# Kernel optimization log

Measured on AMD Instinct MI355X. Metric: run time of the kernel, lower is better.

## Reference

```python
import jax, jax.numpy as jnp
import numpy as np

B, D, H, O, E, R, K, NH = 2048, 512, 2048, 512, 8, 4, 2, 8
DH = O // NH
EPS = 1e-5

def _ln(x, g, b):
    m = x.mean(-1, keepdims=True)
    v = ((x - m) ** 2).mean(-1, keepdims=True)
    return (x - m) / jnp.sqrt(v + EPS) * g + b

def setup_inputs():
    key = jax.random.key(0)
    ks = jax.random.split(key, 16)
    n = lambda k, shape, fan: jax.random.normal(k, shape, jnp.float32) * (fan ** -0.5)
    x = jax.random.normal(ks[0], (B, D), jnp.float32)
    regime = jax.random.randint(ks[1], (B,), 0, R)
    regime_features = jax.nn.one_hot(regime, R, dtype=jnp.float32)
    return dict(
        x=x, regime=regime, regime_features=regime_features,
        ew1=n(ks[2], (R, E, D, H), D), eb1=jnp.zeros((R, E, H)),
        lng=jnp.ones((R, E, H)), lnb=jnp.zeros((R, E, H)),
        ew2=n(ks[3], (R, E, H, O), H), eb2=jnp.zeros((R, E, O)),
        rw1=n(ks[4], (R, D + R, H), D + R), rb1=jnp.zeros((R, H)),
        rw2=n(ks[5], (R, H, E), H), rb2=jnp.zeros((R, E)),
        ipw=n(ks[6], (3 * O, O), O), ipb=jnp.zeros((3 * O,)),
        opw=n(ks[7], (O, O), O), opb=jnp.zeros((O,)),
        ang=jnp.ones((O,)), anb=jnp.zeros((O,)),
    )

def _forward(x, regime, regime_features, ew1, eb1, lng, lnb, ew2, eb2, rw1, rb1, rw2, rb2, ipw, ipb, opw, opb, ang, anb):
    B_ = x.shape[0]
    bi = jnp.arange(B_)
    # regime-conditioned routing: compute logits for all regimes densely, select per sample
    ri = jnp.concatenate([x, regime_features], axis=-1)                  # [B, D+R]
    rh = jax.nn.relu(jnp.einsum('bf,rfh->rbh', ri, rw1) + rb1[:, None])
    logits = (jnp.einsum('rbh,rhe->rbe', rh, rw2) + rb2[:, None])[regime, bi]  # [B, E]
    w = jax.nn.softmax(logits, axis=-1)
    tkw, tki = jax.lax.top_k(w, K)
    tkw = tkw / tkw.sum(-1, keepdims=True)
    # experts: all regimes x all experts, then select the per-sample regime block
    h = jnp.einsum('bd,redh->rebh', x, ew1) + eb1[:, :, None]            # [R, E, B, H]
    h = jax.nn.relu(_ln(h, lng[:, :, None], lnb[:, :, None]))
    eo = jnp.einsum('rebh,reho->rebo', h, ew2) + eb2[:, :, None] + x[None, None]  # identity residual (D == O)
    eo = eo.transpose(0, 2, 1, 3)[regime, bi]                            # [B, E, O]
    # group attention over expert axis (torch MultiheadAttention, eval mode)
    qkv = eo @ ipw.T + ipb
    q, k, v = jnp.split(qkv, 3, axis=-1)
    sh = lambda t: t.reshape(B_, E, NH, DH).transpose(0, 2, 1, 3)
    q, k, v = sh(q), sh(k), sh(v)
    attn = jax.nn.softmax(jnp.einsum('bhqd,bhkd->bhqk', q, k) / np.sqrt(DH).astype(np.float32), axis=-1)
    av = jnp.einsum('bhqk,bhkd->bhqd', attn, v).transpose(0, 2, 1, 3).reshape(B_, E, O)
    eo = _ln(eo + av @ opw.T + opb, ang, anb)
    # top-k combine
    gathered = jnp.take_along_axis(eo, tki[:, :, None], axis=1)          # [B, K, O]
    return jnp.sum(tkw[:, :, None] * gathered, axis=1)

def reference(x, regime, regime_features, ew1, eb1, lng, lnb, ew2, eb2, rw1, rb1, rw2, rb2, ipw, ipb, opw, opb, ang, anb):
    return _forward(x, regime, regime_features, ew1, eb1, lng, lnb, ew2, eb2, rw1, rb1, rw2, rb2, ipw, ipb, opw, opb, ang, anb)
```

## Files before the change

kernel.cpp:

```cpp
#include <hip/hip_runtime.h>
#include <hip/hip_bf16.h>
#include <cstddef>

typedef __attribute__((ext_vector_type(8))) short short8;
typedef __attribute__((ext_vector_type(4))) float f32x4;

constexpr int CB = 2048;
constexpr int CD = 512;
constexpr int CH = 2048;
constexpr int CO = 512;
constexpr int CE = 8;
constexpr int CR = 4;

__device__ __forceinline__ float bs2f(short s){
  union { float f; unsigned u; } u; u.u = ((unsigned)(unsigned short)s) << 16; return u.f;
}
__device__ __forceinline__ short f2bs(float x){
  union { __hip_bfloat16 h; short s; } u; u.h = __float2bfloat16(x); return u.s;
}

#define GLL(g, l) __builtin_amdgcn_global_load_lds((const __attribute__((address_space(1))) void*)(g), (__attribute__((address_space(3))) void*)(l), 16, 0, 0)

__device__ __forceinline__ void block_reduce2(float& a, float& b){
#pragma unroll
  for (int off = 32; off; off >>= 1){ a += __shfl_xor(a, off, 64); b += __shfl_xor(b, off, 64); }
  __shared__ float sa[4], sb[4];
  const int wid = threadIdx.x >> 6, lane = threadIdx.x & 63;
  __syncthreads();
  if (lane == 0){ sa[wid] = a; sb[wid] = b; }
  __syncthreads();
  a = sa[0] + sa[1] + sa[2] + sa[3];
  b = sb[0] + sb[1] + sb[2] + sb[3];
}

__global__ void k_count(const int* __restrict__ regime, int* __restrict__ meta){
  int b = blockIdx.x * 256 + threadIdx.x;
  if (b < CB) atomicAdd(&meta[8 + regime[b]], 1);
}
__global__ void k_scan(int* meta){
  if (threadIdx.x == 0){
    int c0 = meta[8], c1 = meta[9], c2 = meta[10], c3 = meta[11];
    meta[0] = 0; meta[1] = c0; meta[2] = c0 + c1; meta[3] = c0 + c1 + c2; meta[4] = c0 + c1 + c2 + c3;
  }
}
__global__ void k_scatter(const int* __restrict__ regime, int* __restrict__ meta, int* __restrict__ perm){
  int b = blockIdx.x * 256 + threadIdx.x;
  if (b < CB){
    int r = regime[b];
    int pos = atomicAdd(&meta[12 + r], 1);
    perm[meta[r] + pos] = b;
  }
}

__global__ __launch_bounds__(256) void k_xsplit(const float* __restrict__ x, const int* __restrict__ perm,
                                                short* __restrict__ xp, short* __restrict__ xd){
  const int i = blockIdx.x;
  const int b = perm[i];
  const int c = threadIdx.x * 2;
  float2 v = *(const float2*)(x + (size_t)b * CD + c);
  short2 hi; hi.x = f2bs(v.x); hi.y = f2bs(v.y);
  short2 lo; lo.x = f2bs(v.x - bs2f(hi.x)); lo.y = f2bs(v.y - bs2f(hi.y));
  *(short2*)(xp + (size_t)i * CD + c) = hi;
  short* row = xd + (size_t)i * 1536;
  *(short2*)(row + c) = hi;
  *(short2*)(row + 512 + c) = hi;
  *(short2*)(row + 1024 + c) = lo;
}

__global__ __launch_bounds__(256) void k_cvt2(const float* __restrict__ a, short* __restrict__ ao, int na,
                                              const float* __restrict__ b, short* __restrict__ bo, int nb){
  int i = (blockIdx.x * 256 + threadIdx.x) * 8;
  const float* src; short* dst;
  if (i < na){ src = a + i; dst = ao + i; }
  else { int j = i - na; if (j >= nb) return; src = b + j; dst = bo + j; }
  float4 u = *(const float4*)(src);
  float4 v = *(const float4*)(src + 4);
  short8 o;
  o[0]=f2bs(u.x); o[1]=f2bs(u.y); o[2]=f2bs(u.z); o[3]=f2bs(u.w);
  o[4]=f2bs(v.x); o[5]=f2bs(v.y); o[6]=f2bs(v.z); o[7]=f2bs(v.w);
  *(short8*)(dst) = o;
}

__global__ __launch_bounds__(256) void k_cvt_t(const float* __restrict__ in, short* __restrict__ outp, int K, int N){
  __shared__ float tile[64][65];
  const int z = blockIdx.z;
  const int k0 = blockIdx.y * 64, n0 = blockIdx.x * 64;
  const float* src = in + (size_t)z * K * N;
  short* dst = outp + (size_t)z * K * N;
  const int t = threadIdx.x;
  const int kk = t >> 4, nq = (t & 15) * 4;
#pragma unroll
  for (int j = 0; j < 4; j++){
    float4 v = *(const float4*)(src + (size_t)(k0 + kk + j * 16) * N + n0 + nq);
    tile[kk + j * 16][nq] = v.x; tile[kk + j * 16][nq + 1] = v.y;
    tile[kk + j * 16][nq + 2] = v.z; tile[kk + j * 16][nq + 3] = v.w;
  }
  __syncthreads();
  const int n = t >> 2, kq = (t & 3) * 16;
  short8 o0, o1;
#pragma unroll
  for (int j = 0; j < 8; j++) o0[j] = f2bs(tile[kq + j][n]);
#pragma unroll
  for (int j = 0; j < 8; j++) o1[j] = f2bs(tile[kq + 8 + j][n]);
  short* drow = dst + (size_t)(n0 + n) * K + k0 + kq;
  *(short8*)(drow) = o0;
  *(short8*)(drow + 8) = o1;
}

__global__ __launch_bounds__(256) void k_rwt(const float* __restrict__ rw1, const float* __restrict__ rb1,
                                             short* __restrict__ Bp, float* __restrict__ rbias){
  __shared__ float tile[64][65];
  const int r = blockIdx.z;
  const int k0 = blockIdx.y * 64, n0 = blockIdx.x * 64;
  const float* src = rw1 + (size_t)r * (CD + CR) * CH;
  short* dst = Bp + (size_t)r * CH * 1536;
  const int t = threadIdx.x;
  if (blockIdx.y == 0 && t < 64){
    const int n = n0 + t;
    rbias[r * CH + n] = rb1[(size_t)r * CH + n] + src[((size_t)(CD + r)) * CH + n];
  }
  const int kk = t >> 4, nq = (t & 15) * 4;
#pragma unroll
  for (int j = 0; j < 4; j++){
    float4 v = *(const float4*)(src + (size_t)(k0 + kk + j * 16) * CH + n0 + nq);
    tile[kk + j * 16][nq] = v.x; tile[kk + j * 16][nq + 1] = v.y;
    tile[kk + j * 16][nq + 2] = v.z; tile[kk + j * 16][nq + 3] = v.w;
  }
  __syncthreads();
  const int n = t >> 2, kq = (t & 3) * 16;
  short8 h0, h1, l0, l1;
#pragma unroll
  for (int j = 0; j < 8; j++){
    float f = tile[kq + j][n];
    short h = f2bs(f); h0[j] = h; l0[j] = f2bs(f - bs2f(h));
  }
#pragma unroll
  for (int j = 0; j < 8; j++){
    float f = tile[kq + 8 + j][n];
    short h = f2bs(f); h1[j] = h; l1[j] = f2bs(f - bs2f(h));
  }
  short* drow = dst + (size_t)(n0 + n) * 1536;
  *(short8*)(drow + k0 + kq) = h0;        *(short8*)(drow + k0 + kq + 8) = h1;
  *(short8*)(drow + 512 + k0 + kq) = l0;  *(short8*)(drow + 512 + k0 + kq + 8) = l1;
  *(short8*)(drow + 1024 + k0 + kq) = h0; *(short8*)(drow + 1024 + k0 + kq + 8) = h1;
}

__global__ __launch_bounds__(256) void k_logits2(
    const float* __restrict__ part, const float* __restrict__ rb2,
    const int* __restrict__ meta, const int* __restrict__ perm,
    int* __restrict__ tki, float* __restrict__ tkw, int* __restrict__ qrows){
  const int wid = threadIdx.x >> 6, lane = threadIdx.x & 63;
  const int i = blockIdx.x * 4 + wid;
  const int r = (i >= meta[1]) + (i >= meta[2]) + (i >= meta[3]);
  const int p0 = lane >> 3, e = lane & 7;
  float v = 0.f;
#pragma unroll
  for (int j = 0; j < 4; j++)
    v += part[((size_t)(p0 + 8 * j) * CB + i) * 8 + e];
  v += __shfl_xor(v, 8, 64);
  v += __shfl_xor(v, 16, 64);
  v += __shfl_xor(v, 32, 64);
  v += rb2[r * CE + e];
  float l8[8];
#pragma unroll
  for (int e2 = 0; e2 < 8; e2++) l8[e2] = __shfl(v, e2, 64);
  if (lane == 0){
    int i1 = 0; float m1 = l8[0];
#pragma unroll
    for (int e2 = 1; e2 < 8; e2++) if (l8[e2] > m1){ m1 = l8[e2]; i1 = e2; }
    int i2 = -1; float m2 = -1e30f;
#pragma unroll
    for (int e2 = 0; e2 < 8; e2++) if (e2 != i1 && l8[e2] > m2){ m2 = l8[e2]; i2 = e2; }
    const float e2w = __expf(m2 - m1);
    const float w1 = 1.f / (1.f + e2w);
    const int b = perm[i];
    tki[b * 2] = i1; tki[b * 2 + 1] = i2;
    tkw[b * 2] = w1; tkw[b * 2 + 1] = e2w * w1;
    qrows[b * 2] = b * CE + i1; qrows[b * 2 + 1] = b * CE + i2;
  }
}

template<int EPI, bool SWZ>
__global__ __launch_bounds__(256) void gemm_bf16(
    const short* __restrict__ A, long lda,
    const short* __restrict__ Wt, long ldw,
    const int* __restrict__ goff, int fixedM, int Ksub, int ksplit, int N,
    const float* __restrict__ bias, long bstride,
    short* __restrict__ outb, float* __restrict__ outf,
    const int* __restrict__ operm, const float* __restrict__ xtra, int mbs, int nbs){
  constexpr int BK = 32;
  __shared__ __align__(16) short lds[2][8192];

  int bx, by, bz;
  if constexpr (SWZ){
    const int s = blockIdx.x;
    const int chunk = gridDim.x >> 3;
    const int l = (s & 7) * chunk + (s >> 3);
    bx = l % nbs; const int t2 = l / nbs; by = t2 % mbs; bz = t2 / mbs;
  } else { bx = blockIdx.x; by = blockIdx.y; bz = blockIdx.z; }

  const int ks = bz % ksplit;
  const int z = bz / ksplit;
  int g0 = 0, Mg = fixedM;
  if (goff){ const int r = (EPI == 6) ? z : (z >> 3); g0 = goff[r]; Mg = goff[r + 1] - g0; }
  const int m0 = by * 128;
  if (m0 >= Mg) return;
  const int n0 = bx * 128;
  const int e = z & 7;
  const long kbase = (long)ks * Ksub;

  const short* Ab;
  if constexpr (EPI == 2) Ab = A + ((size_t)e * CB + g0) * (size_t)lda;
  else if constexpr (EPI == 1 || EPI == 6) Ab = A + (size_t)g0 * (size_t)lda;
  else Ab = A;
  const short* Wb = Wt + (size_t)z * (size_t)N * (size_t)ldw;

  const int tid = threadIdx.x;
  const int lane = tid & 63, wid = tid >> 6;
  const int srow = lane >> 2;
  const int sc = (((lane & 3) ^ ((srow >> 1) & 3)) << 3);

  int ar0 = m0 + wid * 32 + srow;
  int ar1 = ar0 + 16;
  if (ar0 > Mg - 1) ar0 = Mg - 1;
  if (ar1 > Mg - 1) ar1 = Mg - 1;
  if constexpr (EPI == 3){
    if (operm){ ar0 = operm[ar0]; ar1 = operm[ar1]; }
  }
  const short* ga0 = Ab + (size_t)ar0 * lda + kbase + sc;
  const short* ga1 = Ab + (size_t)ar1 * lda + kbase + sc;
  const int brow = n0 + wid * 32 + srow;
  const short* gb0 = Wb + (size_t)brow * ldw + kbase + sc;
  const short* gb1 = gb0 + (size_t)16 * ldw;

  const int wm = (wid >> 1) * 64, wn = (wid & 1) * 64;
  const int r16 = lane & 15, kb = lane >> 4;
  const int rsw = (r16 >> 1) & 3;

  f32x4 acc[4][4];
#pragma unroll
  for (int a = 0; a < 4; a++)
#pragma unroll
    for (int b = 0; b < 4; b++) acc[a][b] = (f32x4){0.f, 0.f, 0.f, 0.f};

  const int NT = Ksub / BK;
  int buf = 0;

  {
    short* dA = &lds[0][0] + wid * 1024;
    short* dB = &lds[0][4096] + wid * 1024;
    GLL(ga0, dA); GLL(ga1, dA + 512);
    GLL(gb0, dB); GLL(gb1, dB + 512);
  }
  __syncthreads();

  for (int t = 0; t < NT; ++t){
    if (t + 1 < NT){
      const int kof = (t + 1) * BK;
      short* dA = &lds[buf ^ 1][0] + wid * 1024;
      short* dB = &lds[buf ^ 1][4096] + wid * 1024;
      GLL(ga0 + kof, dA); GLL(ga1 + kof, dA + 512);
      GLL(gb0 + kof, dB); GLL(gb1 + kof, dB + 512);
    }
    const short* sA = &lds[buf][0];
    const short* sB = &lds[buf][4096];
    short8 af[4], bfv[4];
#pragma unroll
    for (int mi = 0; mi < 4; mi++)
      af[mi] = *(const short8*)(sA + (wm + mi * 16 + r16) * 32 + ((kb ^ rsw) << 3));
#pragma unroll
    for (int ni = 0; ni < 4; ni++)
      bfv[ni] = *(const short8*)(sB + (wn + ni * 16 + r16) * 32 + ((kb ^ rsw) << 3));
#pragma unroll
    for (int mi = 0; mi < 4; mi++)
#pragma unroll
      for (int ni = 0; ni < 4; ni++)
        acc[mi][ni] = __builtin_amdgcn_mfma_f32_16x16x32_bf16(af[mi], bfv[ni], acc[mi][ni], 0, 0, 0);
    __syncthreads();
    buf ^= 1;
  }

  if constexpr (EPI == 6){
    const int hbase = n0 + wn;
    float wv[4][8]; float rbv[4];
#pragma unroll
    for (int ni = 0; ni < 4; ni++){
      const int h = hbase + ni * 16 + r16;
      rbv[ni] = bias[(size_t)z * CH + h];
      const float* wp = xtra + ((size_t)z * CH + h) * 8;
#pragma unroll
      for (int e2 = 0; e2 < 8; e2++) wv[ni][e2] = wp[e2];
    }
    const int slot = bx * 2 + (wid & 1);
#pragma unroll
    for (int mi = 0; mi < 4; mi++){
#pragma unroll
      for (int q = 0; q < 4; q++){
        float tmp[8];
#pragma unroll
        for (int e2 = 0; e2 < 8; e2++) tmp[e2] = 0.f;
#pragma unroll
        for (int ni = 0; ni < 4; ni++){
          const float v = fmaxf(acc[mi][ni][q] + rbv[ni], 0.f);
#pragma unroll
          for (int e2 = 0; e2 < 8; e2++) tmp[e2] += v * wv[ni][e2];
        }
#pragma unroll
        for (int e2 = 0; e2 < 8; e2++){
          tmp[e2] += __shfl_xor(tmp[e2], 1, 64);
          tmp[e2] += __shfl_xor(tmp[e2], 2, 64);
          tmp[e2] += __shfl_xor(tmp[e2], 4, 64);
          tmp[e2] += __shfl_xor(tmp[e2], 8, 64);
        }
        const int row = wm + mi * 16 + kb * 4 + q;
        if (r16 == 0 && m0 + row < Mg){
          float* dp = outf + ((size_t)slot * CB + (g0 + m0 + row)) * 8;
#pragma unroll
          for (int e2 = 0; e2 < 8; e2++) dp[e2] = tmp[e2];
        }
      }
    }
    return;
  }

#pragma unroll
  for (int mi = 0; mi < 4; mi++){
#pragma unroll
    for (int q = 0; q < 4; q++){
      const int i = m0 + wm + mi * 16 + kb * 4 + q;
      if (i >= Mg) continue;
#pragma unroll
      for (int ni = 0; ni < 4; ni++){
        const int n = n0 + wn + ni * 16 + r16;
        float v = acc[mi][ni][q];
        if constexpr (EPI == 1){
          v += bias[(size_t)z * bstride + n];
          outb[((size_t)e * CB + (g0 + i)) * (size_t)N + n] = f2bs(v);
        } else if constexpr (EPI == 2){
          const int borig = operm[g0 + i];
          outb[(size_t)ks * bstride + ((size_t)borig * CE + e) * (size_t)CO + n] = f2bs(v);
        } else if constexpr (EPI == 3){
          v += bias[n];
          outb[(size_t)i * (size_t)N + n] = f2bs(v);
        } else {
          v += bias[n];
          outf[(size_t)i * (size_t)N + n] = v;
        }
      }
    }
  }
}

__global__ __launch_bounds__(256) void k_eo(const short* __restrict__ P, long pstr,
    const float* __restrict__ eb2, const float* __restrict__ x, const int* __restrict__ regime,
    short* __restrict__ eo){
  const int b = blockIdx.x, e = blockIdx.y;
  const int r = regime[b];
  const int c = threadIdx.x * 2;
  const size_t idx = (((size_t)b * CE + e) << 9) + c;
  short2 a0 = *(const short2*)(P + idx);
  short2 a1 = *(const short2*)(P + pstr + idx);
  short2 a2 = *(const short2*)(P + 2 * pstr + idx);
  short2 a3 = *(const short2*)(P + 3 * pstr + idx);
  float2 xr = *(const float2*)(x + (size_t)b * CD + c);
  float2 eb = *(const float2*)(eb2 + (((size_t)r * CE + e) << 9) + c);
  short2 o;
  o.x = f2bs(bs2f(a0.x) + bs2f(a1.x) + bs2f(a2.x) + bs2f(a3.x) + xr.x + eb.x);
  o.y = f2bs(bs2f(a0.y) + bs2f(a1.y) + bs2f(a2.y) + bs2f(a3.y) + xr.y + eb.y);
  *(short2*)(eo + idx) = o;
}

__global__ __launch_bounds__(256) void k_ln(short* __restrict__ hact,
    const float* __restrict__ lng, const float* __restrict__ lnb, const int* __restrict__ meta){
  const int rowid = blockIdx.x;
  const int e = rowid >> 11, i = rowid & (CB - 1);
  const int r = (i >= meta[1]) + (i >= meta[2]) + (i >= meta[3]);
  short* p = hact + (size_t)rowid * CH;
  short8 raw = *(short8*)(p + threadIdx.x * 8);
  float v[8]; float s = 0.f, sq = 0.f;
#pragma unroll
  for (int j = 0; j < 8; j++){ v[j] = bs2f(raw[j]); s += v[j]; sq += v[j] * v[j]; }
  block_reduce2(s, sq);
  const float mean = s * (1.f / CH);
  const float var = sq * (1.f / CH) - mean * mean;
  const float rstd = rsqrtf(fmaxf(var, 0.f) + 1e-5f);
  const float* g = lng + ((size_t)r * CE + e) * CH;
  const float* bb = lnb + ((size_t)r * CE + e) * CH;
  short8 outv;
#pragma unroll
  for (int j = 0; j < 8; j++){
    const int h = threadIdx.x * 8 + j;
    const float val = (v[j] - mean) * rstd * g[h] + bb[h];
    outv[j] = f2bs(fmaxf(val, 0.f));
  }
  *(short8*)(p + threadIdx.x * 8) = outv;
}

__global__ __launch_bounds__(128) void k_attn(const short* __restrict__ qb, const short* __restrict__ kv,
    const int* __restrict__ tki, short* __restrict__ av){
  const int b = blockIdx.x;
  const int j = threadIdx.x >> 6, d = threadIdx.x & 63;
  const short* q = qb + (size_t)(b * 2 + j) * CO;
  const short* base = kv + (size_t)b * CE * 1024;
#pragma unroll
  for (int h = 0; h < 8; h++){
    const float qv = bs2f(q[h * 64 + d]);
    float sc[8];
#pragma unroll
    for (int e = 0; e < 8; e++){
      float pp = qv * bs2f(base[(size_t)e * 1024 + h * 64 + d]);
#pragma unroll
      for (int off = 32; off; off >>= 1) pp += __shfl_xor(pp, off, 64);
      sc[e] = pp * 0.125f;
    }
    float m = sc[0];
#pragma unroll
    for (int e = 1; e < 8; e++) m = fmaxf(m, sc[e]);
    float den = 0.f, avd = 0.f;
#pragma unroll
    for (int e = 0; e < 8; e++){
      const float pe = __expf(sc[e] - m);
      den += pe;
      avd += pe * bs2f(base[(size_t)e * 1024 + 512 + h * 64 + d]);
    }
    av[((size_t)b * 2 + j) * CO + h * 64 + d] = f2bs(avd / den);
  }
}

__global__ __launch_bounds__(256) void k_final(const short* __restrict__ eo,
    const float* __restrict__ proj, const int* __restrict__ tki, const float* __restrict__ tkw,
    const float* __restrict__ ang, const float* __restrict__ anb, float* __restrict__ out){
  const int b = blockIdx.x, t = threadIdx.x;
  float o0 = 0.f, o1 = 0.f;
#pragma unroll
  for (int j = 0; j < 2; j++){
    const int s = tki[b * 2 + j];
    const float w = tkw[b * 2 + j];
    const short* ep = eo + ((size_t)b * CE + s) * CO;
    const float* pp = proj + ((size_t)b * 2 + j) * CO;
    const float v0 = bs2f(ep[t]) + pp[t];
    const float v1 = bs2f(ep[t + 256]) + pp[t + 256];
    float sm = v0 + v1, sq = v0 * v0 + v1 * v1;
    block_reduce2(sm, sq);
    const float mean = sm * (1.f / CO);
    const float rstd = rsqrtf(fmaxf(sq * (1.f / CO) - mean * mean, 0.f) + 1e-5f);
    o0 += w * ((v0 - mean) * rstd * ang[t] + anb[t]);
    o1 += w * ((v1 - mean) * rstd * ang[t + 256] + anb[t + 256]);
  }
  out[(size_t)b * CO + t] = o0;
  out[(size_t)b * CO + t + 256] = o1;
}

extern "C" void kernel_launch(void* const* d_in, const int* in_sizes, int n_in,
                              void* d_out, int out_size, void* d_ws, size_t ws_size,
                              hipStream_t stream){
  const float* x    = (const float*)d_in[0];
  const int*   regime = (const int*)d_in[1];
  const float* ew1  = (const float*)d_in[3];
  const float* eb1  = (const float*)d_in[4];
  const float* lng  = (const float*)d_in[5];
  const float* lnb  = (const float*)d_in[6];
  const float* ew2  = (const float*)d_in[7];
  const float* eb2  = (const float*)d_in[8];
  const float* rw1  = (const float*)d_in[9];
  const float* rb1  = (const float*)d_in[10];
  const float* rw2  = (const float*)d_in[11];
  const float* rb2  = (const float*)d_in[12];
  const float* ipw  = (const float*)d_in[13];
  const float* ipb  = (const float*)d_in[14];
  const float* opw  = (const float*)d_in[15];
  const float* opb  = (const float*)d_in[16];
  const float* ang  = (const float*)d_in[17];
  const float* anb  = (const float*)d_in[18];
  float* out = (float*)d_out;

  char* ws = (char*)d_ws;
  int*   meta  = (int*)(ws);
  int*   perm  = (int*)(ws + (16u << 10));
  int*   tki   = (int*)(ws + (32u << 10));
  float* tkw   = (float*)(ws + (48u << 10));
  int*   qrows = (int*)(ws + (64u << 10));
  float* rbias = (float*)(ws + (80u << 10));
  short* ipwb  = (short*)(ws + (256u << 10));
  short* opwb  = (short*)(ws + (1792u << 10));
  short* xp    = (short*)(ws + (2304u << 10));
  short* eo    = (short*)(ws + (4352u << 10));
  short* hact  = (short*)(ws + (22ull << 20));
  short* qkv   = (short*)(ws + (22ull << 20));
  short* qb    = (short*)(ws + (54ull << 20));
  short* av    = (short*)(ws + (58ull << 20));
  float* proj  = (float*)(ws + (62ull << 20));
  float* part  = (float*)(ws + (70ull << 20));
  short* wt    = (short*)(ws + (86ull << 20));
  short* P     = (short*)(ws + (150ull << 20));
  short* xd    = (short*)(ws + (216ull << 20));
  const long PSTR = (long)CB * CE * CO;

  hipMemsetAsync(meta, 0, 1024, stream);
  k_count  <<<8, 256, 0, stream>>>(regime, meta);
  k_scan   <<<1, 64, 0, stream>>>(meta);
  k_scatter<<<8, 256, 0, stream>>>(regime, meta, perm);
  k_xsplit <<<CB, 256, 0, stream>>>(x, perm, xp, xd);
  k_cvt2   <<<512, 256, 0, stream>>>(ipw, ipwb, 1536 * 512, opw, opwb, 512 * 512);

  k_rwt<<<dim3(32, 8, CR), 256, 0, stream>>>(rw1, rb1, wt, rbias);
  gemm_bf16<6, false><<<dim3(16, 16, CR), 256, 0, stream>>>(
      xd, 1536, wt, 1536, meta, 0, 1536, 1, CH, rbias, 0,
      nullptr, part, nullptr, rw2, 0, 0);
  k_logits2<<<CB / 4, 256, 0, stream>>>(part, rb2, meta, perm, tki, tkw, qrows);

  k_cvt_t<<<dim3(32, 8, 32), 256, 0, stream>>>(ew1, wt, CD, CH);
  gemm_bf16<1, true><<<8192, 256, 0, stream>>>(
      xp, CD, wt, CD, meta, 0, CD, 1, CH, eb1, CH, hact, nullptr, nullptr, nullptr, 16, 16);
  k_ln<<<CE * CB, 256, 0, stream>>>(hact, lng, lnb, meta);

  k_cvt_t<<<dim3(8, 32, 32), 256, 0, stream>>>(ew2, wt, CH, CO);
  gemm_bf16<2, true><<<8192, 256, 0, stream>>>(
      hact, CH, wt, CH, meta, 0, 512, 4, CO, nullptr, PSTR, P, nullptr, perm, nullptr, 16, 4);
  k_eo<<<dim3(CB, CE), 256, 0, stream>>>(P, PSTR, eb2, x, regime, eo);

  gemm_bf16<3, true><<<1024, 256, 0, stream>>>(
      eo, CO, ipwb + (size_t)512 * 512, CO, nullptr, CB * CE, CO, 1, 1024, ipb + 512, 0,
      qkv, nullptr, nullptr, nullptr, 128, 8);
  gemm_bf16<3, false><<<dim3(4, 32, 1), 256, 0, stream>>>(
      eo, CO, ipwb, CO, nullptr, CB * 2, CO, 1, CO, ipb, 0,
      qb, nullptr, qrows, nullptr, 0, 0);

  k_attn<<<CB, 128, 0, stream>>>(qb, qkv, tki, av);

  gemm_bf16<4, false><<<dim3(4, 32, 1), 256, 0, stream>>>(
      av, CO, opwb, CO, nullptr, CB * 2, CO, 1, CO, opb, 0,
      nullptr, proj, nullptr, nullptr, 0, 0);

  k_final<<<CB, 256, 0, stream>>>(eo, proj, tki, tkw, ang, anb, out);
  (void)in_sizes; (void)n_in; (void)out_size; (void)ws_size;
}
```

Baseline: 449.1 us.

## Fuse expert LayerNorm into GEMM1 stats epilogue and GEMM2 A-operand prologue

The first expert GEMM now computes per-row partial sums and sums of squares in its epilogue and writes them to a stats buffer. A new GEMM2 kernel reduces these partials into mean and rstd, then applies LayerNorm and ReLU on the fly while staging hidden activations into LDS. This removes the standalone LayerNorm pass, which read and rewrote the full hidden tensor. The split-K for GEMM2 also drops from 4 to 2, so k_eo sums fewer partials. In exchange, the A-operand is loaded through registers instead of async global-to-LDS copies and normalised in the inner loop, and variance now comes from E[x²]-mean² over bf16-rounded partials.

```diff
diff --git a/kernel.cpp b/kernel.cpp
--- a/kernel.cpp
+++ b/kernel.cpp
@@ -20,6 +20,19 @@
 }
 
 #define GLL(g, l) __builtin_amdgcn_global_load_lds((const __attribute__((address_space(1))) void*)(g), (__attribute__((address_space(3))) void*)(l), 16, 0, 0)
+
+__device__ __forceinline__ short8 ln8(short8 raw, float mean, float rstd,
+                                      float4 g01, float4 g23, float4 b01, float4 b23){
+  const float g[8] = {g01.x,g01.y,g01.z,g01.w,g23.x,g23.y,g23.z,g23.w};
+  const float b[8] = {b01.x,b01.y,b01.z,b01.w,b23.x,b23.y,b23.z,b23.w};
+  short8 o;
+#pragma unroll
+  for (int j = 0; j < 8; j++){
+    const float v = (bs2f(raw[j]) - mean) * rstd * g[j] + b[j];
+    o[j] = f2bs(fmaxf(v, 0.f));
+  }
+  return o;
+}
 
 __device__ __forceinline__ void block_reduce2(float& a, float& b){
 #pragma unroll
@@ -184,10 +197,11 @@
 __global__ __launch_bounds__(256) void gemm_bf16(
     const short* __restrict__ A, long lda,
     const short* __restrict__ Wt, long ldw,
-    const int* __restrict__ goff, int fixedM, int Ksub, int ksplit, int N,
+    const int* __restrict__ goff, int fixedM, int Ksub, int N,
     const float* __restrict__ bias, long bstride,
     short* __restrict__ outb, float* __restrict__ outf,
-    const int* __restrict__ operm, const float* __restrict__ xtra, int mbs, int nbs){
+    const int* __restrict__ operm, const float* __restrict__ xtra,
+    int mbs, int nbs, float* __restrict__ pstat){
   constexpr int BK = 32;
   __shared__ __align__(16) short lds[2][8192];
 
@@ -199,19 +213,16 @@
     bx = l % nbs; const int t2 = l / nbs; by = t2 % mbs; bz = t2 / mbs;
   } else { bx = blockIdx.x; by = blockIdx.y; bz = blockIdx.z; }
 
-  const int ks = bz % ksplit;
-  const int z = bz / ksplit;
+  const int z = bz;
   int g0 = 0, Mg = fixedM;
   if (goff){ const int r = (EPI == 6) ? z : (z >> 3); g0 = goff[r]; Mg = goff[r + 1] - g0; }
   const int m0 = by * 128;
   if (m0 >= Mg) return;
   const int n0 = bx * 128;
   const int e = z & 7;
-  const long kbase = (long)ks * Ksub;
 
   const short* Ab;
-  if constexpr (EPI == 2) Ab = A + ((size_t)e * CB + g0) * (size_t)lda;
-  else if constexpr (EPI == 1 || EPI == 6) Ab = A + (size_t)g0 * (size_t)lda;
+  if constexpr (EPI == 1 || EPI == 6) Ab = A + (size_t)g0 * (size_t)lda;
   else Ab = A;
   const short* Wb = Wt + (size_t)z * (size_t)N * (size_t)ldw;
 
@@ -227,10 +238,10 @@
   if constexpr (EPI == 3){
     if (operm){ ar0 = operm[ar0]; ar1 = operm[ar1]; }
   }
-  const short* ga0 = Ab + (size_t)ar0 * lda + kbase + sc;
-  const short* ga1 = Ab + (size_t)ar1 * lda + kbase + sc;
+  const short* ga0 = Ab + (size_t)ar0 * lda + sc;
+  const short* ga1 = Ab + (size_t)ar1 * lda + sc;
   const int brow = n0 + wid * 32 + srow;
-  const short* gb0 = Wb + (size_t)brow * ldw + kbase + sc;
+  const short* gb0 = Wb + (size_t)brow * ldw + sc;
   const short* gb1 = gb0 + (size_t)16 * ldw;
 
   const int wm = (wid >> 1) * 64, wn = (wid & 1) * 64;
@@ -278,6 +289,41 @@
         acc[mi][ni] = __builtin_amdgcn_mfma_f32_16x16x32_bf16(af[mi], bfv[ni], acc[mi][ni], 0, 0, 0);
     __syncthreads();
     buf ^= 1;
+  }
+
+  if constexpr (EPI == 1){
+    const int slot = bx * 2 + (wid & 1);
+#pragma unroll
+    for (int mi = 0; mi < 4; mi++){
+#pragma unroll
+      for (int q = 0; q < 4; q++){
+        const int i = m0 + wm + mi * 16 + kb * 4 + q;
+        float vv[4]; float sv = 0.f, sq = 0.f;
+#pragma unroll
+        for (int ni = 0; ni < 4; ni++){
+          const int n = n0 + wn + ni * 16 + r16;
+          const float v = acc[mi][ni][q] + bias[(size_t)z * bstride + n];
+          vv[ni] = v; sv += v; sq += v * v;
+        }
+#pragma unroll
+        for (int off = 1; off < 16; off <<= 1){
+          sv += __shfl_xor(sv, off, 64);
+          sq += __shfl_xor(sq, off, 64);
+        }
+        if (i < Mg){
+#pragma unroll
+          for (int ni = 0; ni < 4; ni++){
+            const int n = n0 + wn + ni * 16 + r16;
+            outb[((size_t)e * CB + (g0 + i)) * (size_t)N + n] = f2bs(vv[ni]);
+          }
+          if (r16 == 0){
+            float* sp = pstat + ((size_t)slot * (CE * CB) + (size_t)e * CB + (g0 + i)) * 2;
+            sp[0] = sv; sp[1] = sq;
+          }
+        }
+      }
+    }
+    return;
   }
 
   if constexpr (EPI == 6){
@@ -332,20 +378,150 @@
 #pragma unroll
       for (int ni = 0; ni < 4; ni++){
         const int n = n0 + wn + ni * 16 + r16;
-        float v = acc[mi][ni][q];
-        if constexpr (EPI == 1){
-          v += bias[(size_t)z * bstride + n];
-          outb[((size_t)e * CB + (g0 + i)) * (size_t)N + n] = f2bs(v);
-        } else if constexpr (EPI == 2){
-          const int borig = operm[g0 + i];
-          outb[(size_t)ks * bstride + ((size_t)borig * CE + e) * (size_t)CO + n] = f2bs(v);
-        } else if constexpr (EPI == 3){
-          v += bias[n];
+        float v = acc[mi][ni][q] + bias[n];
+        if constexpr (EPI == 3){
           outb[(size_t)i * (size_t)N + n] = f2bs(v);
         } else {
-          v += bias[n];
           outf[(size_t)i * (size_t)N + n] = v;
         }
+      }
+    }
+  }
+}
+
+__global__ __launch_bounds__(256) void gemm2_ln(
+    const short* __restrict__ hact, const short* __restrict__ Wt,
+    const int* __restrict__ goff, const float* __restrict__ pstat,
+    const float* __restrict__ lng, const float* __restrict__ lnb,
+    short* __restrict__ P, long pstr, const int* __restrict__ operm){
+  constexpr int BK = 32, KS = 1024;
+  __shared__ __align__(16) short lds[2][8192];
+  __shared__ float smean[128], srstd[128];
+
+  const int s = blockIdx.x;
+  const int chunk = gridDim.x >> 3;
+  const int l = (s & 7) * chunk + (s >> 3);
+  const int bx = l & 3; const int t2 = l >> 2; const int by = t2 & 15; const int bz = t2 >> 4;
+  const int ks = bz & 1, z = bz >> 1;
+  const int r = z >> 3, e = z & 7;
+  const int g0 = goff[r], Mg = goff[r + 1] - g0;
+  const int m0 = by * 128;
+  if (m0 >= Mg) return;
+  const int n0 = bx * 128;
+  const long kbase = (long)ks * KS;
+
+  const int tid = threadIdx.x, lane = tid & 63, wid = tid >> 6;
+
+  if (tid < 128){
+    int lr = m0 + tid; if (lr > Mg - 1) lr = Mg - 1;
+    const size_t rid = (size_t)e * CB + g0 + lr;
+    float S = 0.f, Q = 0.f;
+#pragma unroll
+    for (int p = 0; p < 32; p++){
+      const float2 pp = *(const float2*)(pstat + ((size_t)p * (CE * CB) + rid) * 2);
+      S += pp.x; Q += pp.y;
+    }
+    const float mean = S * (1.f / CH);
+    const float var = Q * (1.f / CH) - mean * mean;
+    smean[tid] = mean;
+    srstd[tid] = rsqrtf(fmaxf(var, 0.f) + 1e-5f);
+  }
+
+  const int srow = lane >> 2;
+  const int c = lane & 3;
+  const int dsw = (srow >> 1) & 3;
+
+  const int lr0 = wid * 32 + srow, lr1 = lr0 + 16;
+  const int cr0 = (m0 + lr0 > Mg - 1) ? (Mg - 1 - m0) : lr0;
+  const int cr1 = (m0 + lr1 > Mg - 1) ? (Mg - 1 - m0) : lr1;
+
+  const short* ga0 = hact + ((size_t)e * CB + g0 + (m0 + cr0)) * (size_t)CH + kbase + c * 8;
+  const short* ga1 = hact + ((size_t)e * CB + g0 + (m0 + cr1)) * (size_t)CH + kbase + c * 8;
+  const float* gp = lng + (size_t)(r * CE + e) * CH + kbase + c * 8;
+  const float* bp = lnb + (size_t)(r * CE + e) * CH + kbase + c * 8;
+
+  const short* Wb = Wt + (size_t)z * (size_t)CO * (size_t)CH;
+  const int brow = n0 + wid * 32 + srow;
+  const int scB = ((c ^ dsw) << 3);
+  const short* gb0 = Wb + (size_t)brow * CH + kbase + scB;
+  const short* gb1 = gb0 + (size_t)16 * CH;
+
+  const int wof0 = lr0 * 32 + ((c ^ dsw) << 3);
+  const int wof1 = lr1 * 32 + ((c ^ dsw) << 3);
+
+  __syncthreads();
+  const float mean0 = smean[cr0], rstd0 = srstd[cr0];
+  const float mean1 = smean[cr1], rstd1 = srstd[cr1];
+
+  const int wm = (wid >> 1) * 64, wn = (wid & 1) * 64;
+  const int r16 = lane & 15, kb = lane >> 4;
+  const int rsw = (r16 >> 1) & 3;
+
+  f32x4 acc[4][4];
+#pragma unroll
+  for (int a = 0; a < 4; a++)
+#pragma unroll
+    for (int b = 0; b < 4; b++) acc[a][b] = (f32x4){0.f, 0.f, 0.f, 0.f};
+
+  const int NT = KS / BK;
+  int buf = 0;
+
+  {
+    short8 a0 = *(const short8*)(ga0);
+    short8 a1 = *(const short8*)(ga1);
+    float4 g01 = *(const float4*)(gp), g23 = *(const float4*)(gp + 4);
+    float4 b01 = *(const float4*)(bp), b23 = *(const float4*)(bp + 4);
+    short* dB = &lds[0][4096] + wid * 1024;
+    GLL(gb0, dB); GLL(gb1, dB + 512);
+    *(short8*)(&lds[0][0] + wof0) = ln8(a0, mean0, rstd0, g01, g23, b01, b23);
+    *(short8*)(&lds[0][0] + wof1) = ln8(a1, mean1, rstd1, g01, g23, b01, b23);
+  }
+  __syncthreads();
+
+  for (int t = 0; t < NT; ++t){
+    short8 na0, na1; float4 ng01, ng23, nb01, nb23;
+    if (t + 1 < NT){
+      const int kof = (t + 1) * BK;
+      na0 = *(const short8*)(ga0 + kof);
+      na1 = *(const short8*)(ga1 + kof);
+      ng01 = *(const float4*)(gp + kof); ng23 = *(const float4*)(gp + kof + 4);
+      nb01 = *(const float4*)(bp + kof); nb23 = *(const float4*)(bp + kof + 4);
+      short* dB = &lds[buf ^ 1][4096] + wid * 1024;
+      GLL(gb0 + kof, dB); GLL(gb1 + kof, dB + 512);
+    }
+    const short* sA = &lds[buf][0];
+    const short* sB = &lds[buf][4096];
+    short8 af[4], bfv[4];
+#pragma unroll
+    for (int mi = 0; mi < 4; mi++)
+      af[mi] = *(const short8*)(sA + (wm + mi * 16 + r16) * 32 + ((kb ^ rsw) << 3));
+#pragma unroll
+    for (int ni = 0; ni < 4; ni++)
+      bfv[ni] = *(const short8*)(sB + (wn + ni * 16 + r16) * 32 + ((kb ^ rsw) << 3));
+#pragma unroll
+    for (int mi = 0; mi < 4; mi++)
+#pragma unroll
+      for (int ni = 0; ni < 4; ni++)
+        acc[mi][ni] = __builtin_amdgcn_mfma_f32_16x16x32_bf16(af[mi], bfv[ni], acc[mi][ni], 0, 0, 0);
+    if (t + 1 < NT){
+      *(short8*)(&lds[buf ^ 1][0] + wof0) = ln8(na0, mean0, rstd0, ng01, ng23, nb01, nb23);
+      *(short8*)(&lds[buf ^ 1][0] + wof1) = ln8(na1, mean1, rstd1, ng01, ng23, nb01, nb23);
+    }
+    __syncthreads();
+    buf ^= 1;
+  }
+
+#pragma unroll
+  for (int mi = 0; mi < 4; mi++){
+#pragma unroll
+    for (int q = 0; q < 4; q++){
+      const int i = m0 + wm + mi * 16 + kb * 4 + q;
+      if (i >= Mg) continue;
+      const int borig = operm[g0 + i];
+#pragma unroll
+      for (int ni = 0; ni < 4; ni++){
+        const int n = n0 + wn + ni * 16 + r16;
+        P[(size_t)ks * pstr + ((size_t)borig * CE + e) * (size_t)CO + n] = f2bs(acc[mi][ni][q]);
       }
     }
   }
@@ -360,40 +536,12 @@
   const size_t idx = (((size_t)b * CE + e) << 9) + c;
   short2 a0 = *(const short2*)(P + idx);
   short2 a1 = *(const short2*)(P + pstr + idx);
-  short2 a2 = *(const short2*)(P + 2 * pstr + idx);
-  short2 a3 = *(const short2*)(P + 3 * pstr + idx);
   float2 xr = *(const float2*)(x + (size_t)b * CD + c);
   float2 eb = *(const float2*)(eb2 + (((size_t)r * CE + e) << 9) + c);
   short2 o;
-  o.x = f2bs(bs2f(a0.x) + bs2f(a1.x) + bs2f(a2.x) + bs2f(a3.x) + xr.x + eb.x);
-  o.y = f2bs(bs2f(a0.y) + bs2f(a1.y) + bs2f(a2.y) + bs2f(a3.y) + xr.y + eb.y);
+  o.x = f2bs(bs2f(a0.x) + bs2f(a1.x) + xr.x + eb.x);
+  o.y = f2bs(bs2f(a0.y) + bs2f(a1.y) + xr.y + eb.y);
   *(short2*)(eo + idx) = o;
-}
-
-__global__ __launch_bounds__(256) void k_ln(short* __restrict__ hact,
-    const float* __restrict__ lng, const float* __restrict__ lnb, const int* __restrict__ meta){
-  const int rowid = blockIdx.x;
-  const int e = rowid >> 11, i = rowid & (CB - 1);
-  const int r = (i >= meta[1]) + (i >= meta[2]) + (i >= meta[3]);
-  short* p = hact + (size_t)rowid * CH;
-  short8 raw = *(short8*)(p + threadIdx.x * 8);
-  float v[8]; float s = 0.f, sq = 0.f;
-#pragma unroll
-  for (int j = 0; j < 8; j++){ v[j] = bs2f(raw[j]); s += v[j]; sq += v[j] * v[j]; }
-  block_reduce2(s, sq);
-  const float mean = s * (1.f / CH);
-  const float var = sq * (1.f / CH) - mean * mean;
-  const float rstd = rsqrtf(fmaxf(var, 0.f) + 1e-5f);
-  const float* g = lng + ((size_t)r * CE + e) * CH;
-  const float* bb = lnb + ((size_t)r * CE + e) * CH;
-  short8 outv;
-#pragma unroll
-  for (int j = 0; j < 8; j++){
-    const int h = threadIdx.x * 8 + j;
-    const float val = (v[j] - mean) * rstd * g[h] + bb[h];
-    outv[j] = f2bs(fmaxf(val, 0.f));
-  }
-  *(short8*)(p + threadIdx.x * 8) = outv;
 }
 
 __global__ __launch_bounds__(128) void k_attn(const short* __restrict__ qb, const short* __restrict__ kv,
@@ -494,6 +642,7 @@
   short* wt    = (short*)(ws + (86ull << 20));
   short* P     = (short*)(ws + (150ull << 20));
   short* xd    = (short*)(ws + (216ull << 20));
+  float* pstat = (float*)(ws + (224ull << 20));
   const long PSTR = (long)CB * CE * CO;
 
   hipMemsetAsync(meta, 0, 1024, stream);
@@ -505,32 +654,30 @@
 
   k_rwt<<<dim3(32, 8, CR), 256, 0, stream>>>(rw1, rb1, wt, rbias);
   gemm_bf16<6, false><<<dim3(16, 16, CR), 256, 0, stream>>>(
-      xd, 1536, wt, 1536, meta, 0, 1536, 1, CH, rbias, 0,
-      nullptr, part, nullptr, rw2, 0, 0);
+      xd, 1536, wt, 1536, meta, 0, 1536, CH, rbias, 0,
+      nullptr, part, nullptr, rw2, 0, 0, nullptr);
   k_logits2<<<CB / 4, 256, 0, stream>>>(part, rb2, meta, perm, tki, tkw, qrows);
 
   k_cvt_t<<<dim3(32, 8, 32), 256, 0, stream>>>(ew1, wt, CD, CH);
   gemm_bf16<1, true><<<8192, 256, 0, stream>>>(
-      xp, CD, wt, CD, meta, 0, CD, 1, CH, eb1, CH, hact, nullptr, nullptr, nullptr, 16, 16);
-  k_ln<<<CE * CB, 256, 0, stream>>>(hact, lng, lnb, meta);
+      xp, CD, wt, CD, meta, 0, CD, CH, eb1, CH, hact, nullptr, nullptr, nullptr, 16, 16, pstat);
 
   k_cvt_t<<<dim3(8, 32, 32), 256, 0, stream>>>(ew2, wt, CH, CO);
-  gemm_bf16<2, true><<<8192, 256, 0, stream>>>(
-      hact, CH, wt, CH, meta, 0, 512, 4, CO, nullptr, PSTR, P, nullptr, perm, nullptr, 16, 4);
+  gemm2_ln<<<4096, 256, 0, stream>>>(hact, wt, meta, pstat, lng, lnb, P, PSTR, perm);
   k_eo<<<dim3(CB, CE), 256, 0, stream>>>(P, PSTR, eb2, x, regime, eo);
 
   gemm_bf16<3, true><<<1024, 256, 0, stream>>>(
-      eo, CO, ipwb + (size_t)512 * 512, CO, nullptr, CB * CE, CO, 1, 1024, ipb + 512, 0,
-      qkv, nullptr, nullptr, nullptr, 128, 8);
+      eo, CO, ipwb + (size_t)512 * 512, CO, nullptr, CB * CE, CO, 1024, ipb + 512, 0,
+      qkv, nullptr, nullptr, nullptr, 128, 8, nullptr);
   gemm_bf16<3, false><<<dim3(4, 32, 1), 256, 0, stream>>>(
-      eo, CO, ipwb, CO, nullptr, CB * 2, CO, 1, CO, ipb, 0,
-      qb, nullptr, qrows, nullptr, 0, 0);
+      eo, CO, ipwb, CO, nullptr, CB * 2, CO, CO, ipb, 0,
+      qb, nullptr, qrows, nullptr, 0, 0, nullptr);
 
   k_attn<<<CB, 128, 0, stream>>>(qb, qkv, tki, av);
 
   gemm_bf16<4, false><<<dim3(4, 32, 1), 256, 0, stream>>>(
-      av, CO, opwb, CO, nullptr, CB * 2, CO, 1, CO, opb, 0,
-      nullptr, proj, nullptr, nullptr, 0, 0);
+      av, CO, opwb, CO, nullptr, CB * 2, CO, CO, opb, 0,
+      nullptr, proj, nullptr, nullptr, 0, 0, nullptr);
 
   k_final<<<CB, 256, 0, stream>>>(eo, proj, tki, tkw, ang, anb, out);
   (void)in_sizes; (void)n_in; (void)out_size; (void)ws_size;
```

New measurement: 448.7 us. About the same (-0.1%).
